# Performance work log

Hardware: AMD Instinct MI355X
Metric: run time of the kernel (lower is better)

Reference implementation:

```python
import jax, jax.numpy as jnp
from jax import lax
import numpy as np

KERNEL_NUM = 6
KERNEL_SIZES = [3 + 2 * i for i in range(KERNEL_NUM)]  # 3,5,7,9,11,13
DN = ('NCHW', 'OIHW', 'NCHW')


def _conv3x3(x, W, b):
    y = lax.conv_general_dilated(x, W, (1, 1), [(1, 1), (1, 1)], dimension_numbers=DN)
    return y + b[None, :, None, None]


def _box_sum(x, k):
    # x: (N, 1, H, W); all-ones kxk conv with zero padding (k-1)//2, as in convSs[i]
    p = (k - 1) // 2
    kern = jnp.ones((1, 1, k, k), x.dtype)
    return lax.conv_general_dilated(x, kern, (1, 1), [(p, p), (p, p)], dimension_numbers=DN)


def _gamma(x):
    # bmfr_gamma_correction: clamp to >=0, then pow(1/2.2)
    return jnp.power(jnp.maximum(x, 0.0), jnp.float32(1.0 / 2.2))


def setup_inputs() -> dict:
    key = jax.random.key(0)
    ks = jax.random.split(key, 7)
    B, C, H, W = 2, 10, 1080, 1920
    s = 0.1
    return {
        'x_in': jax.random.uniform(ks[0], (B, C, H, W), jnp.float32),
        'W1': jax.random.normal(ks[1], (14, 10, 3, 3), jnp.float32) * s,
        'b1': jnp.zeros((14,), jnp.float32),
        'W2': jax.random.normal(ks[2], (14, 14, 3, 3), jnp.float32) * s,
        'b2': jnp.zeros((14,), jnp.float32),
        'W3': jax.random.normal(ks[3], (12, 14, 3, 3), jnp.float32) * s,
        'b3': jnp.zeros((12,), jnp.float32),
    }


def reference(x_in, W1, b1, W2, b2, W3, b3):
    irr = x_in[:, 0:3]
    alb = x_in[:, 3:6]
    x_inputs = jnp.concatenate([_gamma(irr * alb), x_in[:, 3:]], axis=1)  # (B,10,H,W)
    # RepVGG([10,14,14,12]) (deploy form): 3x3 convs, ReLU between, linear output
    h = jax.nn.relu(_conv3x3(x_inputs, W1, b1))
    h = jax.nn.relu(_conv3x3(h, W2, b2))
    out = _conv3x3(h, W3, b3)  # (B,12,H,W)
    guide = jnp.exp(out[:, :KERNEL_NUM])           # (B,6,H,W)
    alpha = jax.nn.softmax(out[:, KERNEL_NUM:], axis=1)  # Softmax2d over channels
    B, _, H, W = x_inputs.shape
    x_out = jnp.zeros((B, 3, H, W), x_in.dtype)
    for i, k in enumerate(KERNEL_SIZES):
        g = guide[:, i:i + 1]                                  # (B,1,H,W)
        wsum = _box_sum(g, k)                                  # (B,1,H,W)
        num = _box_sum((g * irr).reshape(-1, 1, H, W), k).reshape(B, 3, H, W)
        x_out = x_out + alpha[:, i:i + 1] * (num / wsum)
    return x_out * alb
```

## Files before the change

### kernel.cpp

```cpp
#include <hip/hip_runtime.h>
#include <math.h>

namespace {

constexpr int BATCH = 2;
constexpr int H = 1080;
constexpr int W = 1920;
constexpr int HW = H * W;
constexpr int PL = BATCH * HW;
constexpr int NTH = 256;

constexpr int BX = 128;
constexpr int BY = 8;
constexpr int LW = 132;
constexpr int LH = 10;
constexpr int LDSN = LW * LH;
constexpr int NSTG = (LDSN + NTH - 1) / NTH;

constexpr int RMAX = 6;
constexpr int SW_B = 240;
constexpr int COLS = SW_B + 2 * RMAX;
constexpr int SH_B = 12;

__device__ __forceinline__ float gamma22(float v) {
    return v > 0.f ? exp2f(0.45454545454545453f * log2f(v)) : 0.f;
}

template<int CIN, int COUT, bool GAMMA, bool RELU, bool HEAD>
__global__ __launch_bounds__(NTH) void conv4_k(
        const float* __restrict__ in, const float* __restrict__ wgt,
        const float* __restrict__ bias, float* __restrict__ out)
{
    __shared__ float tile[LDSN];

    const int tx = threadIdx.x & 31;
    const int ty = threadIdx.x >> 5;
    const int x0 = blockIdx.x * BX;
    const int y0 = blockIdx.y * BY;
    const int b  = blockIdx.z;

    float acc[COUT][4];
#pragma unroll
    for (int co = 0; co < COUT; ++co) {
        float bv = bias[co];
#pragma unroll
        for (int p = 0; p < 4; ++p) acc[co][p] = bv;
    }

    float rg[NSTG];

    auto stage_load = [&](int ci) {
#pragma unroll
        for (int s = 0; s < NSTG; ++s) {
            int i = threadIdx.x + s * NTH;
            float v = 0.f;
            if (i < LDSN) {
                int r = i / LW, c = i - r * LW;
                int gy = y0 + r - 1, gx = x0 + c - 1;
                if (c < 130 && gy >= 0 && gy < H && gx >= 0 && gx < W) {
                    if (GAMMA) {
                        if (ci < 3) {
                            float a  = in[((size_t)b * 10 + ci) * HW + (size_t)gy * W + gx];
                            float al = in[((size_t)b * 10 + ci + 3) * HW + (size_t)gy * W + gx];
                            v = gamma22(a * al);
                        } else {
                            v = in[((size_t)b * 10 + ci) * HW + (size_t)gy * W + gx];
                        }
                    } else {
                        v = in[(size_t)ci * PL + (size_t)b * HW + (size_t)gy * W + gx];
                    }
                }
            }
            rg[s] = v;
        }
    };

    stage_load(0);

    for (int ci = 0; ci < CIN; ++ci) {
        __syncthreads();
#pragma unroll
        for (int s = 0; s < NSTG; ++s) {
            int i = threadIdx.x + s * NTH;
            if (i < LDSN) tile[i] = rg[s];
        }
        __syncthreads();

        if (ci + 1 < CIN) stage_load(ci + 1);

        float v[3][6];
#pragma unroll
        for (int ky = 0; ky < 3; ++ky) {
            int row = (ty + ky) * LW + tx * 4;
            float4 vA = *reinterpret_cast<const float4*>(&tile[row]);
            float4 vB = *reinterpret_cast<const float4*>(&tile[row + 4]);
            v[ky][0] = vA.x; v[ky][1] = vA.y; v[ky][2] = vA.z; v[ky][3] = vA.w;
            v[ky][4] = vB.x; v[ky][5] = vB.y;
        }

#pragma unroll
        for (int ky = 0; ky < 3; ++ky) {
#pragma unroll
            for (int kx = 0; kx < 3; ++kx) {
#pragma unroll
                for (int co = 0; co < COUT; ++co) {
                    float w = wgt[(co * CIN + ci) * 9 + ky * 3 + kx];
#pragma unroll
                    for (int p = 0; p < 4; ++p)
                        acc[co][p] = fmaf(v[ky][p + kx], w, acc[co][p]);
                }
            }
        }
    }

    const int y = y0 + ty;
    const size_t obase = (size_t)b * HW + (size_t)y * W + x0 + tx * 4;

    if (HEAD) {
#pragma unroll
        for (int p = 0; p < 4; ++p) {
#pragma unroll
            for (int c = 0; c < 6; ++c)
                out[(size_t)c * PL + obase + p] = expf(acc[c][p]);
            float m = acc[6][p];
#pragma unroll
            for (int c = 7; c < 12; ++c) m = fmaxf(m, acc[c][p]);
            float e[6]; float s = 0.f;
#pragma unroll
            for (int c = 0; c < 6; ++c) { e[c] = expf(acc[6 + c][p] - m); s += e[c]; }
            float inv = 1.f / s;
#pragma unroll
            for (int c = 0; c < 6; ++c)
                out[(size_t)(6 + c) * PL + obase + p] = e[c] * inv;
        }
    } else {
#pragma unroll
        for (int co = 0; co < COUT; ++co) {
            float4 r;
            r.x = RELU ? fmaxf(acc[co][0], 0.f) : acc[co][0];
            r.y = RELU ? fmaxf(acc[co][1], 0.f) : acc[co][1];
            r.z = RELU ? fmaxf(acc[co][2], 0.f) : acc[co][2];
            r.w = RELU ? fmaxf(acc[co][3], 0.f) : acc[co][3];
            *reinterpret_cast<float4*>(&out[(size_t)co * PL + obase]) = r;
        }
    }
}

__global__ __launch_bounds__(NTH) void box_all_k(
        const float* __restrict__ ga, const float* __restrict__ xin,
        float* __restrict__ outp)
{
    __shared__ float4 vls4[6 * NTH];

    const int t  = threadIdx.x;
    const int x0 = blockIdx.x * SW_B;
    const int y0 = blockIdx.y * SH_B;
    const int b  = blockIdx.z;
    const int x  = x0 - RMAX + t;

    const bool tok = t < COLS;
    const bool xok = tok && x >= 0 && x < W;

    const float* gb = ga + (size_t)b * HW;
    const float* xb = xin + (size_t)b * 10 * HW;

    float vs[6][4];
#pragma unroll
    for (int i = 0; i < 6; ++i)
#pragma unroll
        for (int c = 0; c < 4; ++c) vs[i][c] = 0.f;

#pragma unroll
    for (int r = -RMAX; r <= RMAX; ++r) {
        int yy = y0 + r;
        float g[6], ir[3];
        if (xok && yy >= 0 && yy < H) {
            size_t ro = (size_t)yy * W + x;
#pragma unroll
            for (int i = 0; i < 6; ++i) g[i] = gb[(size_t)i * PL + ro];
#pragma unroll
            for (int c = 0; c < 3; ++c) ir[c] = xb[(size_t)c * HW + ro];
        } else {
#pragma unroll
            for (int i = 0; i < 6; ++i) g[i] = 0.f;
#pragma unroll
            for (int c = 0; c < 3; ++c) ir[c] = 0.f;
        }
#pragma unroll
        for (int i = 0; i < 6; ++i) {
            if (r >= -(i + 1) && r <= (i + 1)) {
                vs[i][0] += g[i];
                vs[i][1] = fmaf(g[i], ir[0], vs[i][1]);
                vs[i][2] = fmaf(g[i], ir[1], vs[i][2]);
                vs[i][3] = fmaf(g[i], ir[2], vs[i][3]);
            }
        }
    }

    for (int dy = 0; dy < SH_B; ++dy) {
        const int y = y0 + dy;

        if (tok) {
#pragma unroll
            for (int i = 0; i < 6; ++i)
                vls4[i * NTH + t] = make_float4(vs[i][0], vs[i][1], vs[i][2], vs[i][3]);
        }
        __syncthreads();

        if (t >= RMAX && t < RMAX + SW_B) {
            float o0 = 0.f, o1 = 0.f, o2 = 0.f;
            size_t ro = (size_t)y * W + x;
#pragma unroll
            for (int i = 0; i < 6; ++i) {
                const int R = i + 1;
                float sw = 0.f, s0 = 0.f, s1 = 0.f, s2 = 0.f;
#pragma unroll
                for (int dx = -R; dx <= R; ++dx) {
                    float4 v = vls4[i * NTH + t + dx];
                    sw += v.x; s0 += v.y; s1 += v.z; s2 += v.w;
                }
                float a  = gb[(size_t)(6 + i) * PL + ro];
                float rw = a / sw;
                o0 = fmaf(s0, rw, o0);
                o1 = fmaf(s1, rw, o1);
                o2 = fmaf(s2, rw, o2);
            }
            size_t o = (size_t)b * 3 * HW + ro;
            outp[o]                  = o0 * xb[(size_t)3 * HW + ro];
            outp[o + HW]             = o1 * xb[(size_t)4 * HW + ro];
            outp[o + (size_t)2 * HW] = o2 * xb[(size_t)5 * HW + ro];
        }
        __syncthreads();

        if (dy + 1 < SH_B && xok) {
#pragma unroll
            for (int i = 0; i < 6; ++i) {
                const int R = i + 1;
                int ya = y + 1 + R;
                int yr = y - R;
                if (ya < H) {
                    size_t ro = (size_t)ya * W + x;
                    float g = gb[(size_t)i * PL + ro];
                    vs[i][0] += g;
                    vs[i][1] = fmaf(g, xb[ro], vs[i][1]);
                    vs[i][2] = fmaf(g, xb[(size_t)HW + ro], vs[i][2]);
                    vs[i][3] = fmaf(g, xb[(size_t)2 * HW + ro], vs[i][3]);
                }
                if (yr >= 0) {
                    size_t ro = (size_t)yr * W + x;
                    float g = gb[(size_t)i * PL + ro];
                    vs[i][0] -= g;
                    vs[i][1] = fmaf(-g, xb[ro], vs[i][1]);
                    vs[i][2] = fmaf(-g, xb[(size_t)HW + ro], vs[i][2]);
                    vs[i][3] = fmaf(-g, xb[(size_t)2 * HW + ro], vs[i][3]);
                }
            }
        }
    }
}

}

extern "C" void kernel_launch(void* const* d_in, const int* in_sizes, int n_in,
                              void* d_out, int out_size, void* d_ws, size_t ws_size,
                              hipStream_t stream)
{
    const float* xin = (const float*)d_in[0];
    const float* W1p = (const float*)d_in[1];
    const float* b1p = (const float*)d_in[2];
    const float* W2p = (const float*)d_in[3];
    const float* b2p = (const float*)d_in[4];
    const float* W3p = (const float*)d_in[5];
    const float* b3p = (const float*)d_in[6];
    float* outp = (float*)d_out;
    float* ws = (float*)d_ws;

    float* h1 = ws;
    float* h2 = ws + (size_t)14 * PL;
    float* ga = ws;

    dim3 blk(NTH);
    dim3 cgrid(W / BX, H / BY, BATCH);
    dim3 bgrid(W / SW_B, H / SH_B, BATCH);

    conv4_k<10, 14, true,  true,  false><<<cgrid, blk, 0, stream>>>(xin, W1p, b1p, h1);
    conv4_k<14, 14, false, true,  false><<<cgrid, blk, 0, stream>>>(h1,  W2p, b2p, h2);
    conv4_k<14, 12, false, false, true ><<<cgrid, blk, 0, stream>>>(h2,  W3p, b3p, ga);

    box_all_k<<<bgrid, blk, 0, stream>>>(ga, xin, outp);
}
```

Measured before the change: 768.2 us.

## Double-buffer conv LDS tiles, precompute staging offsets, prefetch box outputs

The conv kernel now alternates between two LDS tiles, so each input channel needs one barrier instead of two, and the next channel's global loads overlap the FMAs. Staging offsets and bounds checks are computed once per thread instead of per channel. The box-filter kernel loads alpha and albedo before its barrier to hide latency, and its rows per block are halved for more parallelism. That last change increases the redundant halo reads needed to initialise each block's vertical running sums.

```diff
diff --git a/kernel.cpp b/kernel.cpp
--- a/kernel.cpp
+++ b/kernel.cpp
@@ -20,7 +20,7 @@
 constexpr int RMAX = 6;
 constexpr int SW_B = 240;
 constexpr int COLS = SW_B + 2 * RMAX;
-constexpr int SH_B = 12;
+constexpr int SH_B = 6;
 
 __device__ __forceinline__ float gamma22(float v) {
     return v > 0.f ? exp2f(0.45454545454545453f * log2f(v)) : 0.f;
@@ -31,7 +31,7 @@
         const float* __restrict__ in, const float* __restrict__ wgt,
         const float* __restrict__ bias, float* __restrict__ out)
 {
-    __shared__ float tile[LDSN];
+    __shared__ float tile[2][LDSN];
 
     const int tx = threadIdx.x & 31;
     const int ty = threadIdx.x >> 5;
@@ -39,6 +39,17 @@
     const int y0 = blockIdx.y * BY;
     const int b  = blockIdx.z;
 
+    int  soff[NSTG];
+    bool sok[NSTG];
+#pragma unroll
+    for (int s = 0; s < NSTG; ++s) {
+        int i = threadIdx.x + s * NTH;
+        int r = i / LW, c = i - r * LW;
+        int gy = y0 + r - 1, gx = x0 + c - 1;
+        sok[s]  = (i < LDSN) && c < 130 && gy >= 0 && gy < H && gx >= 0 && gx < W;
+        soff[s] = gy * W + gx;
+    }
+
     float acc[COUT][4];
 #pragma unroll
     for (int co = 0; co < COUT; ++co) {
@@ -50,50 +61,43 @@
     float rg[NSTG];
 
     auto stage_load = [&](int ci) {
+        if (GAMMA && ci < 3) {
+            const float* p0 = in + ((size_t)b * 10 + ci) * HW;
+            const float* p1 = in + ((size_t)b * 10 + ci + 3) * HW;
+#pragma unroll
+            for (int s = 0; s < NSTG; ++s)
+                rg[s] = sok[s] ? gamma22(p0[soff[s]] * p1[soff[s]]) : 0.f;
+        } else {
+            const float* p0 = GAMMA ? in + ((size_t)b * 10 + ci) * HW
+                                    : in + (size_t)ci * PL + (size_t)b * HW;
+#pragma unroll
+            for (int s = 0; s < NSTG; ++s)
+                rg[s] = sok[s] ? p0[soff[s]] : 0.f;
+        }
+    };
+
+    auto stage_write = [&](int buf) {
 #pragma unroll
         for (int s = 0; s < NSTG; ++s) {
             int i = threadIdx.x + s * NTH;
-            float v = 0.f;
-            if (i < LDSN) {
-                int r = i / LW, c = i - r * LW;
-                int gy = y0 + r - 1, gx = x0 + c - 1;
-                if (c < 130 && gy >= 0 && gy < H && gx >= 0 && gx < W) {
-                    if (GAMMA) {
-                        if (ci < 3) {
-                            float a  = in[((size_t)b * 10 + ci) * HW + (size_t)gy * W + gx];
-                            float al = in[((size_t)b * 10 + ci + 3) * HW + (size_t)gy * W + gx];
-                            v = gamma22(a * al);
-                        } else {
-                            v = in[((size_t)b * 10 + ci) * HW + (size_t)gy * W + gx];
-                        }
-                    } else {
-                        v = in[(size_t)ci * PL + (size_t)b * HW + (size_t)gy * W + gx];
-                    }
-                }
-            }
-            rg[s] = v;
+            if (i < LDSN) tile[buf][i] = rg[s];
         }
     };
 
     stage_load(0);
+    stage_write(0);
+    __syncthreads();
 
     for (int ci = 0; ci < CIN; ++ci) {
-        __syncthreads();
-#pragma unroll
-        for (int s = 0; s < NSTG; ++s) {
-            int i = threadIdx.x + s * NTH;
-            if (i < LDSN) tile[i] = rg[s];
-        }
-        __syncthreads();
-
         if (ci + 1 < CIN) stage_load(ci + 1);
 
+        const float* tl = tile[ci & 1];
         float v[3][6];
 #pragma unroll
         for (int ky = 0; ky < 3; ++ky) {
             int row = (ty + ky) * LW + tx * 4;
-            float4 vA = *reinterpret_cast<const float4*>(&tile[row]);
-            float4 vB = *reinterpret_cast<const float4*>(&tile[row + 4]);
+            float4 vA = *reinterpret_cast<const float4*>(&tl[row]);
+            float4 vB = *reinterpret_cast<const float4*>(&tl[row + 4]);
             v[ky][0] = vA.x; v[ky][1] = vA.y; v[ky][2] = vA.z; v[ky][3] = vA.w;
             v[ky][4] = vB.x; v[ky][5] = vB.y;
         }
@@ -110,6 +114,11 @@
                         acc[co][p] = fmaf(v[ky][p + kx], w, acc[co][p]);
                 }
             }
+        }
+
+        if (ci + 1 < CIN) {
+            stage_write((ci + 1) & 1);
+            __syncthreads();
         }
     }
 
@@ -160,6 +169,7 @@
 
     const bool tok = t < COLS;
     const bool xok = tok && x >= 0 && x < W;
+    const bool ook = t >= RMAX && t < RMAX + SW_B;
 
     const float* gb = ga + (size_t)b * HW;
     const float* xb = xin + (size_t)b * 10 * HW;
@@ -199,6 +209,15 @@
 
     for (int dy = 0; dy < SH_B; ++dy) {
         const int y = y0 + dy;
+        const size_t ro = (size_t)y * W + x;
+
+        float al[6], ab[3];
+        if (ook) {
+#pragma unroll
+            for (int i = 0; i < 6; ++i) al[i] = gb[(size_t)(6 + i) * PL + ro];
+#pragma unroll
+            for (int c = 0; c < 3; ++c) ab[c] = xb[(size_t)(3 + c) * HW + ro];
+        }
 
         if (tok) {
 #pragma unroll
@@ -207,9 +226,8 @@
         }
         __syncthreads();
 
-        if (t >= RMAX && t < RMAX + SW_B) {
+        if (ook) {
             float o0 = 0.f, o1 = 0.f, o2 = 0.f;
-            size_t ro = (size_t)y * W + x;
 #pragma unroll
             for (int i = 0; i < 6; ++i) {
                 const int R = i + 1;
@@ -219,16 +237,15 @@
                     float4 v = vls4[i * NTH + t + dx];
                     sw += v.x; s0 += v.y; s1 += v.z; s2 += v.w;
                 }
-                float a  = gb[(size_t)(6 + i) * PL + ro];
-                float rw = a / sw;
+                float rw = al[i] / sw;
                 o0 = fmaf(s0, rw, o0);
                 o1 = fmaf(s1, rw, o1);
                 o2 = fmaf(s2, rw, o2);
             }
             size_t o = (size_t)b * 3 * HW + ro;
-            outp[o]                  = o0 * xb[(size_t)3 * HW + ro];
-            outp[o + HW]             = o1 * xb[(size_t)4 * HW + ro];
-            outp[o + (size_t)2 * HW] = o2 * xb[(size_t)5 * HW + ro];
+            outp[o]                  = o0 * ab[0];
+            outp[o + HW]             = o1 * ab[1];
+            outp[o + (size_t)2 * HW] = o2 * ab[2];
         }
         __syncthreads();
 
@@ -239,20 +256,20 @@
                 int ya = y + 1 + R;
                 int yr = y - R;
                 if (ya < H) {
-                    size_t ro = (size_t)ya * W + x;
-                    float g = gb[(size_t)i * PL + ro];
+                    size_t r2 = (size_t)ya * W + x;
+                    float g = gb[(size_t)i * PL + r2];
                     vs[i][0] += g;
-                    vs[i][1] = fmaf(g, xb[ro], vs[i][1]);
-                    vs[i][2] = fmaf(g, xb[(size_t)HW + ro], vs[i][2]);
-                    vs[i][3] = fmaf(g, xb[(size_t)2 * HW + ro], vs[i][3]);
+                    vs[i][1] = fmaf(g, xb[r2], vs[i][1]);
+                    vs[i][2] = fmaf(g, xb[(size_t)HW + r2], vs[i][2]);
+                    vs[i][3] = fmaf(g, xb[(size_t)2 * HW + r2], vs[i][3]);
                 }
                 if (yr >= 0) {
-                    size_t ro = (size_t)yr * W + x;
-                    float g = gb[(size_t)i * PL + ro];
+                    size_t r2 = (size_t)yr * W + x;
+                    float g = gb[(size_t)i * PL + r2];
                     vs[i][0] -= g;
-                    vs[i][1] = fmaf(-g, xb[ro], vs[i][1]);
-                    vs[i][2] = fmaf(-g, xb[(size_t)HW + ro], vs[i][2]);
-                    vs[i][3] = fmaf(-g, xb[(size_t)2 * HW + ro], vs[i][3]);
+                    vs[i][1] = fmaf(-g, xb[r2], vs[i][1]);
+                    vs[i][2] = fmaf(-g, xb[(size_t)HW + r2], vs[i][2]);
+                    vs[i][3] = fmaf(-g, xb[(size_t)2 * HW + r2], vs[i][3]);
                 }
             }
         }
```

After: 809.9 us. 1.05x slower.
